# Kernel tuning notes

Measured on AMD Instinct MI355X. Metric: run time of the kernel, lower is better.

Reference implementation:

```python
import jax, jax.numpy as jnp
import numpy as np

BN_EPS = 1e-5


def setup_inputs() -> dict:
    key = jax.random.key(0)
    ks = jax.random.split(key, 12)
    N, E, H, INV = 100000, 500000, 128, 16
    DIN = 2 * H + INV  # 272
    x_send = jax.random.normal(ks[0], (N, H), dtype=jnp.float32)
    x_rec = jax.random.normal(ks[1], (N, H), dtype=jnp.float32)
    index = jax.random.randint(ks[2], (2, E), 0, N, dtype=jnp.int64)
    edge_attr = jax.random.normal(ks[3], (E, INV), dtype=jnp.float32)
    # message_mlp = BatchNorm1d(272) -> Linear(272,128) -> SiLU  (eval-mode BN)
    bn_gamma = jax.random.normal(ks[4], (DIN,), dtype=jnp.float32) * 0.1 + 1.0
    bn_beta = jax.random.normal(ks[5], (DIN,), dtype=jnp.float32) * 0.1
    bn_mean = jax.random.normal(ks[6], (DIN,), dtype=jnp.float32) * 0.1
    bn_var = jax.random.uniform(ks[7], (DIN,), dtype=jnp.float32) + 0.5
    W1 = jax.random.normal(ks[8], (DIN, H), dtype=jnp.float32) / np.sqrt(DIN)
    b1 = jnp.zeros((H,), dtype=jnp.float32)
    # edge_inf_mlp = Linear(128,1) -> Sigmoid
    W2 = jax.random.normal(ks[9], (H, 1), dtype=jnp.float32) / np.sqrt(H)
    b2 = jnp.zeros((1,), dtype=jnp.float32)
    return {"x_send": x_send, "x_rec": x_rec, "index": index, "edge_attr": edge_attr,
            "bn_gamma": bn_gamma, "bn_beta": bn_beta, "bn_mean": bn_mean, "bn_var": bn_var,
            "W1": W1, "b1": b1, "W2": W2, "b2": b2}


def reference(x_send, x_rec, index, edge_attr, bn_gamma, bn_beta, bn_mean, bn_var, W1, b1, W2, b2):
    idx_send, idx_rec = index[0], index[1]
    # gather + concat -> [E, 2H + INV]
    state = jnp.concatenate((x_send[idx_send], x_rec[idx_rec], edge_attr), axis=1)
    # eval-mode BatchNorm1d
    state = (state - bn_mean) * (bn_gamma * jax.lax.rsqrt(bn_var + BN_EPS)) + bn_beta
    # Linear + SiLU
    messages = jax.nn.silu(state @ W1 + b1)  # [E, H]
    # edge gating: Linear(H,1) + Sigmoid
    edge_weights = jax.nn.sigmoid(messages @ W2 + b2)  # [E, 1]
    # scatter_add aggregation over receiving nodes
    return jax.ops.segment_sum(messages * edge_weights, idx_rec, num_segments=x_rec.shape[0])
```

## Files before the change

kernel.cpp:

```cpp
#include <hip/hip_runtime.h>
#include <hip/hip_bf16.h>
#include <hip/hip_fp16.h>
#include <math.h>

#define HDIM 128
#define INVD 16
#define DIN 272
#define NKT 9

typedef __attribute__((ext_vector_type(4))) float f32x4;
typedef __attribute__((ext_vector_type(8))) short bf16x8;
typedef __attribute__((ext_vector_type(2))) __fp16 fp16x2;

__device__ inline short f2bf(float f) {
    union { float f; unsigned u; } v; v.f = f;
    unsigned r = v.u + 0x7FFFu + ((v.u >> 16) & 1u);
    return (short)(r >> 16);
}

__device__ inline unsigned cvt_pk_bf16(float a, float b) {
    unsigned r;
    asm("v_cvt_pk_bf16_f32 %0, %1, %2" : "=v"(r) : "v"(a), "v"(b));
    return r;
}

__device__ inline float fast_rcp(float x) {
    float r;
    asm("v_rcp_f32 %0, %1" : "=v"(r) : "v"(x));
    return r;
}

template<int MODE>
__global__ __launch_bounds__(512, 2) void etnn_kernel(
    const float* __restrict__ x_send,
    const float* __restrict__ x_rec,
    const int*   __restrict__ index,
    const float* __restrict__ edge_attr,
    const float* __restrict__ bn_gamma,
    const float* __restrict__ bn_beta,
    const float* __restrict__ bn_mean,
    const float* __restrict__ bn_var,
    const float* __restrict__ W1,
    const float* __restrict__ b1,
    const float* __restrict__ W2,
    const float* __restrict__ b2,
    float* __restrict__ out,
    __half* __restrict__ ws,
    int E, int nIter)
{
    __shared__ short btab[NKT * 8 * 64 * 8];
    __shared__ float scl[DIN];
    __shared__ float shf[DIN];
    __shared__ float bias2[2][HDIM];
    __shared__ float biasT[HDIM];

    const int tid = threadIdx.x;
    const int l  = tid & 63;
    const int lr = l & 15;
    const int lg = l >> 4;

    for (int c = tid; c < DIN; c += 512) {
        float sc = bn_gamma[c] * rsqrtf(bn_var[c] + 1e-5f);
        scl[c] = sc;
        shf[c] = bn_beta[c] - bn_mean[c] * sc;
    }
    __syncthreads();

    for (int f = tid; f < NKT * 8 * 64; f += 512) {
        const int kk  = f >> 9;
        const int cb  = (f >> 6) & 7;
        const int ln  = f & 63;
        const int k0  = kk * 32 + (ln >> 4) * 8;
        const int col = cb * 16 + (ln & 15);
        bf16x8 bv;
        #pragma unroll
        for (int j = 0; j < 8; ++j) {
            const int k = k0 + j;
            float v = (k < DIN) ? scl[k] * W1[k * HDIM + col] : 0.f;
            bv[j] = f2bf(v);
        }
        *(bf16x8*)&btab[f * 8] = bv;
    }
    if (tid < 256) {
        const int col  = tid & 127;
        const int half = tid >> 7;
        float s = 0.f;
        for (int k = half * 136; k < half * 136 + 136; ++k)
            s += shf[k] * W1[k * HDIM + col];
        bias2[half][col] = s;
    }
    __syncthreads();
    if (tid < HDIM) biasT[tid] = b1[tid] + bias2[0][tid] + bias2[1][tid];
    __syncthreads();

    float biasv[8], w2v[8];
    #pragma unroll
    for (int cb = 0; cb < 8; ++cb) {
        biasv[cb] = biasT[cb * 16 + lr];
        w2v[cb]   = W2[cb * 16 + lr];
    }
    const float b2v = b2[0];
    const bool evn = !(lr & 1);

    const int gw = blockIdx.x * 8 + (tid >> 6);
    const int NW = gridDim.x * 8;

    for (int it = gw; it < nIter; it += NW) {
        const int e0 = it * 16;
        const int pos = e0 + lr;
        const int pc  = (pos < E) ? pos : E - 1;
        const int is = index[pc];
        const int ir = index[E + pc];

        const f32x4* ps = (const f32x4*)(x_send + (size_t)is * HDIM);
        const f32x4* pr = (const f32x4*)(x_rec  + (size_t)ir * HDIM);
        f32x4 Ls[8], Lr[8], La[2];
        #pragma unroll
        for (int kk = 0; kk < 4; ++kk) {
            Ls[kk * 2]     = ps[kk * 8 + lg * 2];
            Ls[kk * 2 + 1] = ps[kk * 8 + lg * 2 + 1];
            Lr[kk * 2]     = pr[kk * 8 + lg * 2];
            Lr[kk * 2 + 1] = pr[kk * 8 + lg * 2 + 1];
        }
        if (lg < 2) {
            const f32x4* pa = (const f32x4*)(edge_attr + (size_t)pc * INVD + lg * 8);
            La[0] = pa[0]; La[1] = pa[1];
        } else {
            La[0] = (f32x4){0.f, 0.f, 0.f, 0.f};
            La[1] = (f32x4){0.f, 0.f, 0.f, 0.f};
        }

        f32x4 acc[8];
        #pragma unroll
        for (int cb = 0; cb < 8; ++cb) acc[cb] = (f32x4){0.f, 0.f, 0.f, 0.f};

        #pragma unroll
        for (int kk = 0; kk < NKT; ++kk) {
            f32x4 lo = (kk < 4) ? Ls[kk * 2]     : (kk < 8) ? Lr[(kk - 4) * 2]     : La[0];
            f32x4 hi = (kk < 4) ? Ls[kk * 2 + 1] : (kk < 8) ? Lr[(kk - 4) * 2 + 1] : La[1];
            union { bf16x8 v; unsigned u[4]; } a;
            a.u[0] = cvt_pk_bf16(lo[0], lo[1]);
            a.u[1] = cvt_pk_bf16(lo[2], lo[3]);
            a.u[2] = cvt_pk_bf16(hi[0], hi[1]);
            a.u[3] = cvt_pk_bf16(hi[2], hi[3]);
            #pragma unroll
            for (int cb = 0; cb < 8; ++cb) {
                bf16x8 b = *(const bf16x8*)&btab[((kk * 8 + cb) * 64 + l) * 8];
                acc[cb] = __builtin_amdgcn_mfma_f32_16x16x32_bf16(a.v, b, acc[cb], 0, 0, 0);
            }
        }

        float p[4] = {0.f, 0.f, 0.f, 0.f};
        #pragma unroll
        for (int cb = 0; cb < 8; ++cb) {
            #pragma unroll
            for (int q = 0; q < 4; ++q) {
                float z = acc[cb][q] + biasv[cb];
                float m = z * fast_rcp(1.f + __expf(-z));
                acc[cb][q] = m;
                p[q] += m * w2v[cb];
            }
        }
        #pragma unroll
        for (int q = 0; q < 4; ++q) {
            p[q] += __shfl_xor(p[q], 1, 64);
            p[q] += __shfl_xor(p[q], 2, 64);
            p[q] += __shfl_xor(p[q], 4, 64);
            p[q] += __shfl_xor(p[q], 8, 64);
        }

        #pragma unroll
        for (int q = 0; q < 4; ++q) {
            const int row = lg * 4 + q;
            if (e0 + row < E) {
                const int irq = __shfl(ir, row, 64);
                const float g = fast_rcp(1.f + __expf(-(p[q] + b2v)));
                if constexpr (MODE == 1) {
                    float m[8];
                    #pragma unroll
                    for (int cb = 0; cb < 8; ++cb) m[cb] = acc[cb][q] * g;
                    #pragma unroll
                    for (int c = 0; c < 4; ++c) {
                        float x0 = __shfl_xor(m[2 * c],     1, 64);
                        float x1 = __shfl_xor(m[2 * c + 1], 1, 64);
                        float va = evn ? m[2 * c] : x1;
                        float vb = evn ? x0       : m[2 * c + 1];
                        union { fp16x2 h; unsigned u; } pk;
                        pk.h = __builtin_amdgcn_cvt_pkrtz(va, vb);
                        const int col0 = evn ? (32 * c + lr) : (32 * c + 15 + lr);
                        unsigned long long a =
                            (unsigned long long)(ws + (size_t)irq * HDIM + col0);
                        asm volatile("global_atomic_pk_add_f16 %0, %1, off"
                                     :: "v"(a), "v"(pk.u) : "memory");
                    }
                } else {
                    float* orow = out + (size_t)irq * HDIM + lr;
                    #pragma unroll
                    for (int cb = 0; cb < 8; ++cb)
                        atomicAdd(orow + cb * 16, acc[cb][q] * g);
                }
            }
        }
    }
}

__global__ __launch_bounds__(256) void cvt_kernel(const __half* __restrict__ ws,
                                                  float* __restrict__ out, int n) {
    int i = (blockIdx.x * 256 + threadIdx.x) * 4;
    if (i < n) {
        const __half2* p = (const __half2*)(ws + i);
        float2 a = __half22float2(p[0]);
        float2 b = __half22float2(p[1]);
        f32x4 v = {a.x, a.y, b.x, b.y};
        *(f32x4*)(out + i) = v;
    }
}

extern "C" void kernel_launch(void* const* d_in, const int* in_sizes, int n_in,
                              void* d_out, int out_size, void* d_ws, size_t ws_size,
                              hipStream_t stream) {
    const float* x_send    = (const float*)d_in[0];
    const float* x_rec     = (const float*)d_in[1];
    const int*   index     = (const int*)d_in[2];
    const float* edge_attr = (const float*)d_in[3];
    const float* bn_gamma  = (const float*)d_in[4];
    const float* bn_beta   = (const float*)d_in[5];
    const float* bn_mean   = (const float*)d_in[6];
    const float* bn_var    = (const float*)d_in[7];
    const float* W1        = (const float*)d_in[8];
    const float* b1        = (const float*)d_in[9];
    const float* W2        = (const float*)d_in[10];
    const float* b2        = (const float*)d_in[11];
    float* out = (float*)d_out;

    const int E = in_sizes[3] / INVD;
    const int N = in_sizes[0] / HDIM;
    const int nIter = (E + 15) / 16;
    const int grid = 512;

    const size_t accBytes = (size_t)N * HDIM * sizeof(__half);
    if (ws_size >= accBytes) {
        __half* ws = (__half*)d_ws;
        hipMemsetAsync(ws, 0, accBytes, stream);
        etnn_kernel<1><<<grid, 512, 0, stream>>>(x_send, x_rec, index, edge_attr,
                                                 bn_gamma, bn_beta, bn_mean, bn_var,
                                                 W1, b1, W2, b2, out, ws, E, nIter);
        const int n = N * HDIM;
        cvt_kernel<<<(n / 4 + 255) / 256, 256, 0, stream>>>(ws, out, n);
    } else {
        hipMemsetAsync(d_out, 0, (size_t)out_size * sizeof(float), stream);
        etnn_kernel<0><<<grid, 512, 0, stream>>>(x_send, x_rec, index, edge_attr,
                                                 bn_gamma, bn_beta, bn_mean, bn_var,
                                                 W1, b1, W2, b2, out, nullptr, E, nIter);
    }
}
```

Measured before the change: 195.8 us.

## Hoist BN-folded weight packing into a prep kernel and read weights from global

Moves the per-block BatchNorm folding and bf16 packing of W1 into a single-block prep kernel that writes the packed weights and fused bias to workspace. The main kernel then reads MFMA B operands straight from global memory (L2/L1 cached) instead of LDS, and switches to 256-thread blocks with a 2048-block grid and a different launch bound. This removes the redundant per-block prologue and the LDS footprint but adds a serialized tiny kernel launch and relies on cache hits for the weight reads in the inner loop. The fallback path now writes the pack into the workspace even when it is too small.

```diff
diff --git a/kernel.cpp b/kernel.cpp
--- a/kernel.cpp
+++ b/kernel.cpp
@@ -7,6 +7,7 @@
 #define INVD 16
 #define DIN 272
 #define NKT 9
+#define PACKSH (NKT * 8 * 64 * 8)
 
 typedef __attribute__((ext_vector_type(4))) float f32x4;
 typedef __attribute__((ext_vector_type(8))) short bf16x8;
@@ -30,43 +31,25 @@
     return r;
 }
 
-template<int MODE>
-__global__ __launch_bounds__(512, 2) void etnn_kernel(
-    const float* __restrict__ x_send,
-    const float* __restrict__ x_rec,
-    const int*   __restrict__ index,
-    const float* __restrict__ edge_attr,
-    const float* __restrict__ bn_gamma,
-    const float* __restrict__ bn_beta,
-    const float* __restrict__ bn_mean,
-    const float* __restrict__ bn_var,
-    const float* __restrict__ W1,
-    const float* __restrict__ b1,
-    const float* __restrict__ W2,
-    const float* __restrict__ b2,
-    float* __restrict__ out,
-    __half* __restrict__ ws,
-    int E, int nIter)
+__global__ __launch_bounds__(256) void prep_kernel(
+    const float* __restrict__ bn_gamma, const float* __restrict__ bn_beta,
+    const float* __restrict__ bn_mean,  const float* __restrict__ bn_var,
+    const float* __restrict__ W1,       const float* __restrict__ b1,
+    short* __restrict__ W1pack, float* __restrict__ biasTg)
 {
-    __shared__ short btab[NKT * 8 * 64 * 8];
     __shared__ float scl[DIN];
     __shared__ float shf[DIN];
     __shared__ float bias2[2][HDIM];
-    __shared__ float biasT[HDIM];
-
     const int tid = threadIdx.x;
-    const int l  = tid & 63;
-    const int lr = l & 15;
-    const int lg = l >> 4;
-
-    for (int c = tid; c < DIN; c += 512) {
+
+    for (int c = tid; c < DIN; c += 256) {
         float sc = bn_gamma[c] * rsqrtf(bn_var[c] + 1e-5f);
         scl[c] = sc;
         shf[c] = bn_beta[c] - bn_mean[c] * sc;
     }
     __syncthreads();
 
-    for (int f = tid; f < NKT * 8 * 64; f += 512) {
+    for (int f = tid; f < NKT * 8 * 64; f += 256) {
         const int kk  = f >> 9;
         const int cb  = (f >> 6) & 7;
         const int ln  = f & 63;
@@ -79,9 +62,9 @@
             float v = (k < DIN) ? scl[k] * W1[k * HDIM + col] : 0.f;
             bv[j] = f2bf(v);
         }
-        *(bf16x8*)&btab[f * 8] = bv;
-    }
-    if (tid < 256) {
+        *(bf16x8*)&W1pack[f * 8] = bv;
+    }
+    {
         const int col  = tid & 127;
         const int half = tid >> 7;
         float s = 0.f;
@@ -90,20 +73,39 @@
         bias2[half][col] = s;
     }
     __syncthreads();
-    if (tid < HDIM) biasT[tid] = b1[tid] + bias2[0][tid] + bias2[1][tid];
-    __syncthreads();
+    if (tid < HDIM) biasTg[tid] = b1[tid] + bias2[0][tid] + bias2[1][tid];
+}
+
+template<int MODE>
+__global__ __launch_bounds__(256, 4) void etnn_kernel(
+    const float* __restrict__ x_send,
+    const float* __restrict__ x_rec,
+    const int*   __restrict__ index,
+    const float* __restrict__ edge_attr,
+    const float* __restrict__ W2,
+    const float* __restrict__ b2,
+    const short* __restrict__ W1pack,
+    const float* __restrict__ biasTg,
+    float* __restrict__ out,
+    __half* __restrict__ ws,
+    int E, int nIter)
+{
+    const int tid = threadIdx.x;
+    const int l  = tid & 63;
+    const int lr = l & 15;
+    const int lg = l >> 4;
 
     float biasv[8], w2v[8];
     #pragma unroll
     for (int cb = 0; cb < 8; ++cb) {
-        biasv[cb] = biasT[cb * 16 + lr];
+        biasv[cb] = biasTg[cb * 16 + lr];
         w2v[cb]   = W2[cb * 16 + lr];
     }
     const float b2v = b2[0];
     const bool evn = !(lr & 1);
 
-    const int gw = blockIdx.x * 8 + (tid >> 6);
-    const int NW = gridDim.x * 8;
+    const int gw = blockIdx.x * 4 + (tid >> 6);
+    const int NW = gridDim.x * 4;
 
     for (int it = gw; it < nIter; it += NW) {
         const int e0 = it * 16;
@@ -145,7 +147,7 @@
             a.u[3] = cvt_pk_bf16(hi[2], hi[3]);
             #pragma unroll
             for (int cb = 0; cb < 8; ++cb) {
-                bf16x8 b = *(const bf16x8*)&btab[((kk * 8 + cb) * 64 + l) * 8];
+                bf16x8 b = *(const bf16x8*)&W1pack[((kk * 8 + cb) * 64 + l) * 8];
                 acc[cb] = __builtin_amdgcn_mfma_f32_16x16x32_bf16(a.v, b, acc[cb], 0, 0, 0);
             }
         }
@@ -236,21 +238,32 @@
     const int E = in_sizes[3] / INVD;
     const int N = in_sizes[0] / HDIM;
     const int nIter = (E + 15) / 16;
-    const int grid = 512;
-
-    const size_t accBytes = (size_t)N * HDIM * sizeof(__half);
-    if (ws_size >= accBytes) {
-        __half* ws = (__half*)d_ws;
+    const int grid = 2048;
+
+    const size_t accBytes  = (size_t)N * HDIM * sizeof(__half);
+    const size_t accAl     = (accBytes + 255) & ~(size_t)255;
+    const size_t packBytes = (size_t)PACKSH * sizeof(short) + HDIM * sizeof(float);
+
+    if (ws_size >= accAl + packBytes) {
+        __half* ws   = (__half*)d_ws;
+        short* pack  = (short*)((char*)d_ws + accAl);
+        float* biasg = (float*)(pack + PACKSH);
         hipMemsetAsync(ws, 0, accBytes, stream);
-        etnn_kernel<1><<<grid, 512, 0, stream>>>(x_send, x_rec, index, edge_attr,
-                                                 bn_gamma, bn_beta, bn_mean, bn_var,
-                                                 W1, b1, W2, b2, out, ws, E, nIter);
+        prep_kernel<<<1, 256, 0, stream>>>(bn_gamma, bn_beta, bn_mean, bn_var,
+                                           W1, b1, pack, biasg);
+        etnn_kernel<1><<<grid, 256, 0, stream>>>(x_send, x_rec, index, edge_attr,
+                                                 W2, b2, pack, biasg,
+                                                 out, ws, E, nIter);
         const int n = N * HDIM;
         cvt_kernel<<<(n / 4 + 255) / 256, 256, 0, stream>>>(ws, out, n);
     } else {
+        short* pack  = (short*)d_ws;
+        float* biasg = (float*)(pack + PACKSH);
         hipMemsetAsync(d_out, 0, (size_t)out_size * sizeof(float), stream);
-        etnn_kernel<0><<<grid, 512, 0, stream>>>(x_send, x_rec, index, edge_attr,
-                                                 bn_gamma, bn_beta, bn_mean, bn_var,
-                                                 W1, b1, W2, b2, out, nullptr, E, nIter);
-    }
-}
+        prep_kernel<<<1, 256, 0, stream>>>(bn_gamma, bn_beta, bn_mean, bn_var,
+                                           W1, b1, pack, biasg);
+        etnn_kernel<0><<<grid, 256, 0, stream>>>(x_send, x_rec, index, edge_attr,
+                                                 W2, b2, pack, biasg,
+                                                 out, nullptr, E, nIter);
+    }
+}
```

New measurement: 534.1 us. 2.73x slower.

## Halve block size and prefetch next iteration's edge indices

Applied to the files above, without the earlier changes.

Blocks shrink from 512 to 256 threads (4 waves each) with the grid kept at 512, which halves the resident warps and doubles per-warp iterations. Each warp now loads the send/receive indices for its next iteration while the current tile's features are in flight, so the dependent index load no longer sits in front of the gather. An empty asm barrier pins the gathered registers so the compiler cannot sink their loads. The cost is less parallelism for hiding gather latency and a longer per-block setup relative to its work.

```diff
diff --git a/kernel.cpp b/kernel.cpp
--- a/kernel.cpp
+++ b/kernel.cpp
@@ -31,7 +31,7 @@
 }
 
 template<int MODE>
-__global__ __launch_bounds__(512, 2) void etnn_kernel(
+__global__ __launch_bounds__(256, 2) void etnn_kernel(
     const float* __restrict__ x_send,
     const float* __restrict__ x_rec,
     const int*   __restrict__ index,
@@ -59,14 +59,14 @@
     const int lr = l & 15;
     const int lg = l >> 4;
 
-    for (int c = tid; c < DIN; c += 512) {
+    for (int c = tid; c < DIN; c += 256) {
         float sc = bn_gamma[c] * rsqrtf(bn_var[c] + 1e-5f);
         scl[c] = sc;
         shf[c] = bn_beta[c] - bn_mean[c] * sc;
     }
     __syncthreads();
 
-    for (int f = tid; f < NKT * 8 * 64; f += 512) {
+    for (int f = tid; f < NKT * 8 * 64; f += 256) {
         const int kk  = f >> 9;
         const int cb  = (f >> 6) & 7;
         const int ln  = f & 63;
@@ -81,7 +81,7 @@
         }
         *(bf16x8*)&btab[f * 8] = bv;
     }
-    if (tid < 256) {
+    {
         const int col  = tid & 127;
         const int half = tid >> 7;
         float s = 0.f;
@@ -102,15 +102,21 @@
     const float b2v = b2[0];
     const bool evn = !(lr & 1);
 
-    const int gw = blockIdx.x * 8 + (tid >> 6);
-    const int NW = gridDim.x * 8;
+    const int gw = blockIdx.x * 4 + (tid >> 6);
+    const int NW = gridDim.x * 4;
+
+    if (gw >= nIter) return;
+
+    int pc, is, ir;
+    {
+        int pos = gw * 16 + lr;
+        pc = (pos < E) ? pos : E - 1;
+        is = index[pc];
+        ir = index[E + pc];
+    }
 
     for (int it = gw; it < nIter; it += NW) {
         const int e0 = it * 16;
-        const int pos = e0 + lr;
-        const int pc  = (pos < E) ? pos : E - 1;
-        const int is = index[pc];
-        const int ir = index[E + pc];
 
         const f32x4* ps = (const f32x4*)(x_send + (size_t)is * HDIM);
         const f32x4* pr = (const f32x4*)(x_rec  + (size_t)ir * HDIM);
@@ -129,6 +135,23 @@
             La[0] = (f32x4){0.f, 0.f, 0.f, 0.f};
             La[1] = (f32x4){0.f, 0.f, 0.f, 0.f};
         }
+
+        const int irc = ir;
+        {
+            int itn = it + NW;
+            int pos = (itn < nIter) ? itn * 16 + lr : pc;
+            int pcn = (pos < E) ? pos : E - 1;
+            pc = pcn;
+            is = index[pcn];
+            ir = index[E + pcn];
+        }
+
+        asm volatile("" :
+            "+v"(Ls[0]), "+v"(Ls[1]), "+v"(Ls[2]), "+v"(Ls[3]),
+            "+v"(Ls[4]), "+v"(Ls[5]), "+v"(Ls[6]), "+v"(Ls[7]),
+            "+v"(Lr[0]), "+v"(Lr[1]), "+v"(Lr[2]), "+v"(Lr[3]),
+            "+v"(Lr[4]), "+v"(Lr[5]), "+v"(Lr[6]), "+v"(Lr[7]),
+            "+v"(La[0]), "+v"(La[1]));
 
         f32x4 acc[8];
         #pragma unroll
@@ -173,7 +196,7 @@
         for (int q = 0; q < 4; ++q) {
             const int row = lg * 4 + q;
             if (e0 + row < E) {
-                const int irq = __shfl(ir, row, 64);
+                const int irq = __shfl(irc, row, 64);
                 const float g = fast_rcp(1.f + __expf(-(p[q] + b2v)));
                 if constexpr (MODE == 1) {
                     float m[8];
@@ -242,14 +265,14 @@
     if (ws_size >= accBytes) {
         __half* ws = (__half*)d_ws;
         hipMemsetAsync(ws, 0, accBytes, stream);
-        etnn_kernel<1><<<grid, 512, 0, stream>>>(x_send, x_rec, index, edge_attr,
+        etnn_kernel<1><<<grid, 256, 0, stream>>>(x_send, x_rec, index, edge_attr,
                                                  bn_gamma, bn_beta, bn_mean, bn_var,
                                                  W1, b1, W2, b2, out, ws, E, nIter);
         const int n = N * HDIM;
         cvt_kernel<<<(n / 4 + 255) / 256, 256, 0, stream>>>(ws, out, n);
     } else {
         hipMemsetAsync(d_out, 0, (size_t)out_size * sizeof(float), stream);
-        etnn_kernel<0><<<grid, 512, 0, stream>>>(x_send, x_rec, index, edge_attr,
+        etnn_kernel<0><<<grid, 256, 0, stream>>>(x_send, x_rec, index, edge_attr,
                                                  bn_gamma, bn_beta, bn_mean, bn_var,
                                                  W1, b1, W2, b2, out, nullptr, E, nIter);
     }
```

Result: no change. 193.1 us (-1.4%).
